# Kernel optimization log

Hardware: AMD Instinct MI355X
Metric: run time of the kernel (lower is better)

The kernel has to match this reference:

```python
import jax, jax.numpy as jnp
import numpy as np

D_MODEL = 1024
N_HEAD = 16
B, T = 1, 4096


def setup_inputs() -> dict:
    key = jax.random.key(0)
    ks = jax.random.split(key, 12)
    s = 1.0 / np.sqrt(D_MODEL)
    inp = {
        "q": jax.random.normal(ks[0], (B, T, D_MODEL), jnp.float32),
        "k": jax.random.normal(ks[1], (B, T, D_MODEL), jnp.float32),
        "v": jax.random.normal(ks[2], (B, T, D_MODEL), jnp.float32),
        # causal mask: True = keep, False = mask out (mask==0 path in torch)
        "mask": jnp.tril(jnp.ones((T, T), dtype=bool))[None, None],
        "w_q": jax.random.uniform(ks[3], (D_MODEL, D_MODEL), jnp.float32, -s, s),
        "b_q": jax.random.uniform(ks[4], (D_MODEL,), jnp.float32, -s, s),
        "w_k": jax.random.uniform(ks[5], (D_MODEL, D_MODEL), jnp.float32, -s, s),
        "b_k": jax.random.uniform(ks[6], (D_MODEL,), jnp.float32, -s, s),
        "w_v": jax.random.uniform(ks[7], (D_MODEL, D_MODEL), jnp.float32, -s, s),
        "b_v": jax.random.uniform(ks[8], (D_MODEL,), jnp.float32, -s, s),
        "w_o": jax.random.uniform(ks[9], (D_MODEL, D_MODEL), jnp.float32, -s, s),
        "b_o": jax.random.uniform(ks[10], (D_MODEL,), jnp.float32, -s, s),
    }
    return inp


def reference(q, k, v, mask, w_q, b_q, w_k, b_k, w_v, b_v, w_o, b_o):
    batch, time, d_model = q.shape
    n_d = d_model // N_HEAD
    # Linear projections (torch Linear: x @ W.T + b)
    qh = (q @ w_q.T + b_q).reshape(batch, time, N_HEAD, n_d).transpose(0, 2, 1, 3)
    kh = (k @ w_k.T + b_k).reshape(batch, -1, N_HEAD, n_d).transpose(0, 2, 1, 3)
    vh = (v @ w_v.T + b_v).reshape(batch, -1, N_HEAD, n_d).transpose(0, 2, 1, 3)
    # [B, H, Tq, Tk] score matrix (naive, materialized as in original)
    score = jnp.einsum("bhqd,bhkd->bhqk", qh, kh) / jnp.sqrt(jnp.float32(n_d))
    score = jnp.where(mask, score, jnp.float32(-10000.0))
    attn = jax.nn.softmax(score, axis=-1)
    out = jnp.einsum("bhqk,bhkd->bhqd", attn, vh)
    out = out.transpose(0, 2, 1, 3).reshape(batch, time, d_model)
    return out @ w_o.T + b_o
```

## Files before the change

### kernel.cpp

```cpp
#include <hip/hip_runtime.h>

typedef unsigned short u16;
typedef unsigned int u32;
typedef __bf16 b16x8 __attribute__((ext_vector_type(8)));
typedef float f32x4 __attribute__((ext_vector_type(4)));
typedef u32 u32x4 __attribute__((ext_vector_type(4)));

__device__ __forceinline__ u16 f2b(float f) {
    u32 u = __builtin_bit_cast(u32, f);
    u32 r = (u + 0x7fffu + ((u >> 16) & 1u)) >> 16;
    return (u16)r;
}
__device__ __forceinline__ float b2f(u16 h) {
    u32 u = ((u32)h) << 16;
    return __builtin_bit_cast(float, u);
}
__device__ __forceinline__ b16x8 frag(u32x4 x) { return __builtin_bit_cast(b16x8, x); }

__device__ __forceinline__ void gld16(const u16* g, u16* l) {
    __builtin_amdgcn_global_load_lds((const __attribute__((address_space(1))) u32*)g,
                                     (__attribute__((address_space(3))) u32*)l, 16, 0, 0);
}

#define SEQ 4096
#define DMODEL 1024
#define NHEAD 16
#define HDIM 64
#define QK_SCALE 0.18033688011112042f

__global__ void cvt3(const float* __restrict__ s0, const float* __restrict__ s1,
                     const float* __restrict__ s2, u16* __restrict__ d0,
                     u16* __restrict__ d1, u16* __restrict__ d2, int n4) {
    const int t = blockIdx.y;
    const float* s = (t == 0) ? s0 : (t == 1) ? s1 : s2;
    u16* d = (t == 0) ? d0 : (t == 1) ? d1 : d2;
    const int stride = gridDim.x * blockDim.x;
    for (int i = blockIdx.x * blockDim.x + threadIdx.x; i < n4; i += stride) {
        float4 f = ((const float4*)s)[i];
        ushort4 o;
        o.x = f2b(f.x); o.y = f2b(f.y); o.z = f2b(f.z); o.w = f2b(f.w);
        ((ushort4*)d)[i] = o;
    }
}

__global__ void cvt4(const float* __restrict__ s0, const float* __restrict__ s1,
                     const float* __restrict__ s2, const float* __restrict__ s3,
                     u16* __restrict__ d0, u16* __restrict__ d1,
                     u16* __restrict__ d2, u16* __restrict__ d3, int n4) {
    const int t = blockIdx.y;
    const float* s = (t == 0) ? s0 : (t == 1) ? s1 : (t == 2) ? s2 : s3;
    u16* d = (t == 0) ? d0 : (t == 1) ? d1 : (t == 2) ? d2 : d3;
    const int stride = gridDim.x * blockDim.x;
    for (int i = blockIdx.x * blockDim.x + threadIdx.x; i < n4; i += stride) {
        float4 f = ((const float4*)s)[i];
        ushort4 o;
        o.x = f2b(f.x); o.y = f2b(f.y); o.z = f2b(f.z); o.w = f2b(f.w);
        ((ushort4*)d)[i] = o;
    }
}

__global__ __launch_bounds__(256) void gemm_qkv(
    const u16* __restrict__ cq, const u16* __restrict__ ck, const u16* __restrict__ cv,
    const u16* __restrict__ cwq, const u16* __restrict__ cwk, const u16* __restrict__ cwv,
    const float* __restrict__ bq, const float* __restrict__ bk, const float* __restrict__ bv,
    u16* __restrict__ qh, u16* __restrict__ kh, u16* __restrict__ vt) {
    constexpr int K = 1024;
    __shared__ __attribute__((aligned(16))) u16 As[128 * 32];
    __shared__ __attribute__((aligned(16))) u16 Bs[128 * 32];

    const int z = blockIdx.z;
    const u16* A = (z == 0) ? cq : (z == 1) ? ck : cwv;
    const u16* Bt = (z == 0) ? cwq : (z == 1) ? cwk : cv;
    const float* bias = (z == 0) ? bq : (z == 1) ? bk : bv;

    int m0, n0;
    if (z < 2) {
        m0 = blockIdx.y * 128;
        n0 = blockIdx.x * 128;
    } else {
        const int id = blockIdx.y * 8 + blockIdx.x;
        m0 = (id >> 5) * 128;
        n0 = (id & 31) * 128;
    }

    const int tid = threadIdx.x;
    const int wave = tid >> 6, lane = tid & 63;
    const int quad = lane >> 4, l16 = lane & 15;
    const int wr = wave >> 1, wc = wave & 1;

    f32x4 acc[4][4] = {};

    const int srow = tid >> 2;
    const int scol = (tid & 3) * 8;
    const u16* Aptr = A + (size_t)(m0 + srow) * K + scol;
    const u16* Bptr = Bt + (size_t)(n0 + srow) * K + scol;
    u16* AsW0 = &As[wave * 512];
    u16* AsW1 = &As[2048 + wave * 512];
    u16* BsW0 = &Bs[wave * 512];
    u16* BsW1 = &Bs[2048 + wave * 512];

    for (int k0 = 0; k0 < K; k0 += 32) {
        __syncthreads();
        gld16(Aptr + k0, AsW0);
        gld16(Aptr + k0 + (size_t)64 * K, AsW1);
        gld16(Bptr + k0, BsW0);
        gld16(Bptr + k0 + (size_t)64 * K, BsW1);
        __syncthreads();

        b16x8 af[4], bf[4];
#pragma unroll
        for (int mt = 0; mt < 4; ++mt)
            af[mt] = frag(*(const u32x4*)&As[(wr * 64 + mt * 16 + l16) * 32 + quad * 8]);
#pragma unroll
        for (int nt = 0; nt < 4; ++nt)
            bf[nt] = frag(*(const u32x4*)&Bs[(wc * 64 + nt * 16 + l16) * 32 + quad * 8]);
#pragma unroll
        for (int mt = 0; mt < 4; ++mt)
#pragma unroll
            for (int nt = 0; nt < 4; ++nt)
                acc[mt][nt] = __builtin_amdgcn_mfma_f32_16x16x32_bf16(af[mt], bf[nt], acc[mt][nt], 0, 0, 0);
    }

    u16* C = (z == 0) ? qh : kh;
    const float sc = (z == 0) ? QK_SCALE : 1.0f;
#pragma unroll
    for (int nt = 0; nt < 4; ++nt) {
        const int col = n0 + wc * 64 + nt * 16 + l16;
        const float bcol = (z < 2) ? bias[col] : 0.f;
#pragma unroll
        for (int mt = 0; mt < 4; ++mt) {
            const int row0 = m0 + wr * 64 + mt * 16 + quad * 4;
#pragma unroll
            for (int r = 0; r < 4; ++r) {
                const int row = row0 + r;
                float v = acc[mt][nt][r];
                if (z == 2) {
                    v += bias[row];
                    vt[(size_t)row * SEQ + col] = f2b(v);
                } else {
                    v = (v + bcol) * sc;
                    C[((size_t)(col >> 6) * SEQ + row) * HDIM + (col & 63)] = f2b(v);
                }
            }
        }
    }
}

__global__ __launch_bounds__(256) void gemm_out(const u16* __restrict__ A,
                                                const u16* __restrict__ Bt,
                                                const float* __restrict__ bias,
                                                float* __restrict__ C) {
    constexpr int K = 1024, N = 1024;
    __shared__ __attribute__((aligned(16))) u16 As[128 * 32];
    __shared__ __attribute__((aligned(16))) u16 Bs[64 * 32];

    const int tid = threadIdx.x;
    const int wave = tid >> 6, lane = tid & 63;
    const int quad = lane >> 4, l16 = lane & 15;
    const int wr = wave >> 1, wc = wave & 1;
    const int m0 = blockIdx.y * 128, n0 = blockIdx.x * 64;

    f32x4 acc[4][2] = {};

    const int srow = tid >> 2;
    const int scol = (tid & 3) * 8;
    const u16* Aptr = A + (size_t)(m0 + srow) * K + scol;
    const u16* Bptr = Bt + (size_t)(n0 + wave * 16 + (lane >> 2)) * K + (lane & 3) * 8;
    u16* AsW0 = &As[wave * 512];
    u16* AsW1 = &As[2048 + wave * 512];
    u16* BsW = &Bs[wave * 512];

    for (int k0 = 0; k0 < K; k0 += 32) {
        __syncthreads();
        gld16(Aptr + k0, AsW0);
        gld16(Aptr + k0 + (size_t)64 * K, AsW1);
        gld16(Bptr + k0, BsW);
        __syncthreads();

        b16x8 af[4], bf[2];
#pragma unroll
        for (int mt = 0; mt < 4; ++mt)
            af[mt] = frag(*(const u32x4*)&As[(wr * 64 + mt * 16 + l16) * 32 + quad * 8]);
#pragma unroll
        for (int nt = 0; nt < 2; ++nt)
            bf[nt] = frag(*(const u32x4*)&Bs[(wc * 32 + nt * 16 + l16) * 32 + quad * 8]);
#pragma unroll
        for (int mt = 0; mt < 4; ++mt)
#pragma unroll
            for (int nt = 0; nt < 2; ++nt)
                acc[mt][nt] = __builtin_amdgcn_mfma_f32_16x16x32_bf16(af[mt], bf[nt], acc[mt][nt], 0, 0, 0);
    }

#pragma unroll
    for (int nt = 0; nt < 2; ++nt) {
        const int col = n0 + wc * 32 + nt * 16 + l16;
        const float bv = bias[col];
#pragma unroll
        for (int mt = 0; mt < 4; ++mt) {
            const int row0 = m0 + wr * 64 + mt * 16 + quad * 4;
#pragma unroll
            for (int r = 0; r < 4; ++r)
                C[(size_t)(row0 + r) * N + col] = acc[mt][nt][r] + bv;
        }
    }
}

__global__ __launch_bounds__(256) void flash_attn(const u16* __restrict__ Q,
                                                  const u16* __restrict__ K,
                                                  const u16* __restrict__ V,
                                                  u16* __restrict__ pO,
                                                  float* __restrict__ pL) {
    constexpr int LDK = 72;
    __shared__ __attribute__((aligned(16))) u16 Ks[64 * LDK];
    __shared__ __attribute__((aligned(16))) u16 Vs[64 * LDK];
    __shared__ __attribute__((aligned(16))) u16 Ps[128 * LDK];

    const int tid = threadIdx.x;
    const int wave = tid >> 6, lane = tid & 63;
    const int quad = lane >> 4, l16 = lane & 15;

    const int x = blockIdx.x, h = blockIdx.y;
    int qt, c, nc;
    if (x < 8)       { qt = x;                 c = 0;            nc = 1; }
    else if (x < 24) { qt = 8 + ((x - 8) >> 1);  c = (x - 8) & 1;  nc = 2; }
    else if (x < 48) { qt = 16 + (x - 24) / 3;   c = (x - 24) % 3; nc = 3; }
    else             { qt = 24 + ((x - 48) >> 2); c = (x - 48) & 3; nc = 4; }
    const int nkt = 2 * qt + 2;
    const int kt0 = (c * nkt) / nc, kt1 = ((c + 1) * nkt) / nc;
    const int q0 = qt * 128;
    const int slot = h * 80 + x;

    const u16* Qh = Q + (size_t)h * SEQ * HDIM;
    const u16* Kh = K + (size_t)h * SEQ * HDIM;
    const u16* Vh = V + (size_t)h * HDIM * SEQ;

    b16x8 qf[2][2];
#pragma unroll
    for (int mf = 0; mf < 2; ++mf) {
        const u16* qp = Qh + (size_t)(q0 + wave * 32 + mf * 16 + l16) * HDIM + quad * 8;
        qf[mf][0] = frag(*(const u32x4*)qp);
        qf[mf][1] = frag(*(const u32x4*)(qp + 32));
    }
    b16x8 onesf;
    {
        u32x4 o = {0x3F803F80u, 0x3F803F80u, 0x3F803F80u, 0x3F803F80u};
        onesf = frag(o);
    }

    f32x4 acc[2][4] = {};
    f32x4 accl[2] = {};

    const int r0 = tid >> 3;
    const int c0 = (tid & 7) * 8;

    for (int kt = kt0; kt < kt1; ++kt) {
        const int k0 = kt * 64;
        u32x4 ka = *(const u32x4*)(Kh + (size_t)(k0 + r0) * HDIM + c0);
        u32x4 kb = *(const u32x4*)(Kh + (size_t)(k0 + r0 + 32) * HDIM + c0);
        u32x4 va = *(const u32x4*)(Vh + (size_t)r0 * SEQ + k0 + c0);
        u32x4 vb = *(const u32x4*)(Vh + (size_t)(r0 + 32) * SEQ + k0 + c0);
        __syncthreads();
        *(u32x4*)&Ks[r0 * LDK + c0] = ka;
        *(u32x4*)&Ks[(r0 + 32) * LDK + c0] = kb;
        *(u32x4*)&Vs[r0 * LDK + c0] = va;
        *(u32x4*)&Vs[(r0 + 32) * LDK + c0] = vb;
        __syncthreads();

        f32x4 s[2][4];
#pragma unroll
        for (int nt = 0; nt < 4; ++nt) {
            b16x8 kf0 = frag(*(const u32x4*)&Ks[(nt * 16 + l16) * LDK + quad * 8]);
            b16x8 kf1 = frag(*(const u32x4*)&Ks[(nt * 16 + l16) * LDK + 32 + quad * 8]);
#pragma unroll
            for (int mf = 0; mf < 2; ++mf) {
                f32x4 z = {};
                z = __builtin_amdgcn_mfma_f32_16x16x32_bf16(qf[mf][0], kf0, z, 0, 0, 0);
                z = __builtin_amdgcn_mfma_f32_16x16x32_bf16(qf[mf][1], kf1, z, 0, 0, 0);
                s[mf][nt] = z;
            }
        }

        if (kt >= 2 * qt) {
#pragma unroll
            for (int nt = 0; nt < 4; ++nt) {
                const int j = k0 + nt * 16 + l16;
#pragma unroll
                for (int mf = 0; mf < 2; ++mf) {
                    const int ib = q0 + wave * 32 + mf * 16 + quad * 4;
#pragma unroll
                    for (int r = 0; r < 4; ++r)
                        if (j > ib + r) s[mf][nt][r] = -1e30f;
                }
            }
        }

#pragma unroll
        for (int mf = 0; mf < 2; ++mf)
#pragma unroll
            for (int nt = 0; nt < 4; ++nt)
#pragma unroll
                for (int r = 0; r < 4; ++r) {
                    const float p = __builtin_amdgcn_exp2f(s[mf][nt][r] - 16.0f);
                    Ps[(wave * 32 + mf * 16 + quad * 4 + r) * LDK + nt * 16 + l16] = f2b(p);
                }
        __syncthreads();

#pragma unroll
        for (int ks = 0; ks < 2; ++ks) {
            b16x8 a[2];
#pragma unroll
            for (int mf = 0; mf < 2; ++mf) {
                a[mf] = frag(*(const u32x4*)&Ps[(wave * 32 + mf * 16 + l16) * LDK + ks * 32 + quad * 8]);
                accl[mf] = __builtin_amdgcn_mfma_f32_16x16x32_bf16(a[mf], onesf, accl[mf], 0, 0, 0);
            }
#pragma unroll
            for (int dt = 0; dt < 4; ++dt) {
                b16x8 b = frag(*(const u32x4*)&Vs[(dt * 16 + l16) * LDK + ks * 32 + quad * 8]);
#pragma unroll
                for (int mf = 0; mf < 2; ++mf)
                    acc[mf][dt] = __builtin_amdgcn_mfma_f32_16x16x32_bf16(a[mf], b, acc[mf][dt], 0, 0, 0);
            }
        }
    }

    u16* po = pO + (size_t)slot * 8192;
#pragma unroll
    for (int mf = 0; mf < 2; ++mf) {
        const int row0 = wave * 32 + mf * 16 + quad * 4;
#pragma unroll
        for (int dt = 0; dt < 4; ++dt) {
            const int col = dt * 16 + l16;
            ushort4 o;
            o.x = f2b(acc[mf][dt][0]);
            o.y = f2b(acc[mf][dt][1]);
            o.z = f2b(acc[mf][dt][2]);
            o.w = f2b(acc[mf][dt][3]);
            *(ushort4*)&po[col * 128 + row0] = o;
        }
        if (l16 == 0) {
#pragma unroll
            for (int r = 0; r < 4; ++r)
                pL[(size_t)slot * 128 + row0 + r] = accl[mf][r];
        }
    }
}

__global__ __launch_bounds__(256) void combine(const u16* __restrict__ pO,
                                               const float* __restrict__ pL,
                                               u16* __restrict__ att) {
    const int qt = blockIdx.x, h = blockIdx.y;
    const int g = qt >> 3;
    const int nc = g + 1;
    const int slot0 = h * 80 + 4 * g * (g + 1) + (qt - (g << 3)) * nc;

    const int t = threadIdx.x;
    const int row = t >> 1;
    const int ch = (t & 1) * 32;

    float lsum = 0.f;
    for (int cc = 0; cc < nc; ++cc) lsum += pL[(size_t)(slot0 + cc) * 128 + row];
    const float inv = 1.0f / lsum;

    u16 out[32];
#pragma unroll 4
    for (int i = 0; i < 32; ++i) {
        const int col = ch + i;
        float o = 0.f;
        for (int cc = 0; cc < nc; ++cc)
            o += b2f(pO[(size_t)(slot0 + cc) * 8192 + col * 128 + row]);
        out[i] = f2b(o * inv);
    }
    u16* dst = att + (size_t)(qt * 128 + row) * DMODEL + h * HDIM + ch;
#pragma unroll
    for (int i = 0; i < 8; ++i) ((ushort4*)dst)[i] = *(ushort4*)&out[i * 4];
}

extern "C" void kernel_launch(void* const* d_in, const int* in_sizes, int n_in,
                              void* d_out, int out_size, void* d_ws, size_t ws_size,
                              hipStream_t stream) {
    const float* qkv[3] = {nullptr, nullptr, nullptr};
    const float* wts[4] = {nullptr, nullptr, nullptr, nullptr};
    const float* bss[4] = {nullptr, nullptr, nullptr, nullptr};
    int nqkv = 0, nw = 0, nb = 0;
    for (int i = 0; i < n_in; ++i) {
        const int sz = in_sizes[i];
        if (sz == SEQ * DMODEL) {
            if (nqkv < 3) qkv[nqkv++] = (const float*)d_in[i];
        } else if (sz == DMODEL * DMODEL) {
            if (nw < 4) wts[nw++] = (const float*)d_in[i];
        } else if (sz == DMODEL) {
            if (nb < 4) bss[nb++] = (const float*)d_in[i];
        }
    }

    u16* ws = (u16*)d_ws;
    const size_t ELEMS = (size_t)SEQ * DMODEL;
    const size_t WELEMS = (size_t)DMODEL * DMODEL;

    size_t off = 0;
    u16* cq = ws + off; off += ELEMS;
    u16* ck = ws + off; off += ELEMS;
    u16* cv = ws + off; off += ELEMS;
    u16* cwq = ws + off; off += WELEMS;
    u16* cwk = ws + off; off += WELEMS;
    u16* cwv = ws + off; off += WELEMS;
    u16* cwo = ws + off; off += WELEMS;
    u16* qh = ws + off; off += ELEMS;
    u16* kh = ws + off; off += ELEMS;
    u16* vt = ws + off; off += ELEMS;
    u16* att = ws + off; off += ELEMS;
    u16* pO = cq;
    float* pL = (float*)cwq;

    dim3 blk(256);
    cvt3<<<dim3(1024, 3), blk, 0, stream>>>(qkv[0], qkv[1], qkv[2], cq, ck, cv,
                                            (int)(ELEMS / 4));
    cvt4<<<dim3(256, 4), blk, 0, stream>>>(wts[0], wts[1], wts[2], wts[3],
                                           cwq, cwk, cwv, cwo, (int)(WELEMS / 4));

    gemm_qkv<<<dim3(8, 32, 3), blk, 0, stream>>>(cq, ck, cv, cwq, cwk, cwv,
                                                 bss[0], bss[1], bss[2], qh, kh, vt);
    flash_attn<<<dim3(80, NHEAD), blk, 0, stream>>>(qh, kh, vt, pO, pL);
    combine<<<dim3(SEQ / 128, NHEAD), blk, 0, stream>>>(pO, pL, att);
    gemm_out<<<dim3(16, 32), blk, 0, stream>>>(att, cwo, bss[3], (float*)d_out);
}
```

Measured before the change: 368.7 us.

## Double-buffer GEMM LDS tiles, prefetch K/V in attention, reorder attention blocks

The QKV and output GEMMs now use two LDS buffers, so the next 32-wide K slice loads into the second buffer while MFMAs run on the first. This halves the barrier pairs per K step at the cost of twice the shared memory. Flash attention loads the next K/V tile into registers while computing the current one, and drops the barrier after writing P, since each wave reads only its own P rows. Block indices are reversed so the longest causal query tiles are scheduled first, which should reduce tail imbalance.

```diff
diff --git a/kernel.cpp b/kernel.cpp
--- a/kernel.cpp
+++ b/kernel.cpp
@@ -59,14 +59,26 @@
     }
 }
 
+#define GEMM_PHASE(AS, BS)                                                                  \
+    {                                                                                       \
+        b16x8 af[4], bf[4];                                                                 \
+        _Pragma("unroll") for (int mt = 0; mt < 4; ++mt) af[mt] =                           \
+            frag(*(const u32x4*)&(AS)[(wr * 64 + mt * 16 + l16) * 32 + quad * 8]);          \
+        _Pragma("unroll") for (int nt = 0; nt < 4; ++nt) bf[nt] =                           \
+            frag(*(const u32x4*)&(BS)[(wc * 64 + nt * 16 + l16) * 32 + quad * 8]);          \
+        _Pragma("unroll") for (int mt = 0; mt < 4; ++mt)                                    \
+            _Pragma("unroll") for (int nt = 0; nt < 4; ++nt) acc[mt][nt] =                  \
+                __builtin_amdgcn_mfma_f32_16x16x32_bf16(af[mt], bf[nt], acc[mt][nt], 0, 0, 0); \
+    }
+
 __global__ __launch_bounds__(256) void gemm_qkv(
     const u16* __restrict__ cq, const u16* __restrict__ ck, const u16* __restrict__ cv,
     const u16* __restrict__ cwq, const u16* __restrict__ cwk, const u16* __restrict__ cwv,
     const float* __restrict__ bq, const float* __restrict__ bk, const float* __restrict__ bv,
     u16* __restrict__ qh, u16* __restrict__ kh, u16* __restrict__ vt) {
     constexpr int K = 1024;
-    __shared__ __attribute__((aligned(16))) u16 As[128 * 32];
-    __shared__ __attribute__((aligned(16))) u16 Bs[128 * 32];
+    __shared__ __attribute__((aligned(16))) u16 As[2][128 * 32];
+    __shared__ __attribute__((aligned(16))) u16 Bs[2][128 * 32];
 
     const int z = blockIdx.z;
     const u16* A = (z == 0) ? cq : (z == 1) ? ck : cwv;
@@ -94,31 +106,32 @@
     const int scol = (tid & 3) * 8;
     const u16* Aptr = A + (size_t)(m0 + srow) * K + scol;
     const u16* Bptr = Bt + (size_t)(n0 + srow) * K + scol;
-    u16* AsW0 = &As[wave * 512];
-    u16* AsW1 = &As[2048 + wave * 512];
-    u16* BsW0 = &Bs[wave * 512];
-    u16* BsW1 = &Bs[2048 + wave * 512];
-
-    for (int k0 = 0; k0 < K; k0 += 32) {
-        __syncthreads();
-        gld16(Aptr + k0, AsW0);
-        gld16(Aptr + k0 + (size_t)64 * K, AsW1);
-        gld16(Bptr + k0, BsW0);
-        gld16(Bptr + k0 + (size_t)64 * K, BsW1);
-        __syncthreads();
-
-        b16x8 af[4], bf[4];
-#pragma unroll
-        for (int mt = 0; mt < 4; ++mt)
-            af[mt] = frag(*(const u32x4*)&As[(wr * 64 + mt * 16 + l16) * 32 + quad * 8]);
-#pragma unroll
-        for (int nt = 0; nt < 4; ++nt)
-            bf[nt] = frag(*(const u32x4*)&Bs[(wc * 64 + nt * 16 + l16) * 32 + quad * 8]);
-#pragma unroll
-        for (int mt = 0; mt < 4; ++mt)
-#pragma unroll
-            for (int nt = 0; nt < 4; ++nt)
-                acc[mt][nt] = __builtin_amdgcn_mfma_f32_16x16x32_bf16(af[mt], bf[nt], acc[mt][nt], 0, 0, 0);
+    const int woff = wave * 512;
+
+    gld16(Aptr, &As[0][woff]);
+    gld16(Aptr + (size_t)64 * K, &As[0][2048 + woff]);
+    gld16(Bptr, &Bs[0][woff]);
+    gld16(Bptr + (size_t)64 * K, &Bs[0][2048 + woff]);
+
+    for (int k0 = 0; k0 < K; k0 += 64) {
+        __syncthreads();
+        {
+            const int kn = k0 + 32;
+            gld16(Aptr + kn, &As[1][woff]);
+            gld16(Aptr + kn + (size_t)64 * K, &As[1][2048 + woff]);
+            gld16(Bptr + kn, &Bs[1][woff]);
+            gld16(Bptr + kn + (size_t)64 * K, &Bs[1][2048 + woff]);
+        }
+        GEMM_PHASE(As[0], Bs[0]);
+        __syncthreads();
+        if (k0 + 64 < K) {
+            const int kn = k0 + 64;
+            gld16(Aptr + kn, &As[0][woff]);
+            gld16(Aptr + kn + (size_t)64 * K, &As[0][2048 + woff]);
+            gld16(Bptr + kn, &Bs[0][woff]);
+            gld16(Bptr + kn + (size_t)64 * K, &Bs[0][2048 + woff]);
+        }
+        GEMM_PHASE(As[1], Bs[1]);
     }
 
     u16* C = (z == 0) ? qh : kh;
@@ -151,8 +164,8 @@
                                                 const float* __restrict__ bias,
                                                 float* __restrict__ C) {
     constexpr int K = 1024, N = 1024;
-    __shared__ __attribute__((aligned(16))) u16 As[128 * 32];
-    __shared__ __attribute__((aligned(16))) u16 Bs[64 * 32];
+    __shared__ __attribute__((aligned(16))) u16 As[2][128 * 32];
+    __shared__ __attribute__((aligned(16))) u16 Bs[2][64 * 32];
 
     const int tid = threadIdx.x;
     const int wave = tid >> 6, lane = tid & 63;
@@ -166,29 +179,41 @@
     const int scol = (tid & 3) * 8;
     const u16* Aptr = A + (size_t)(m0 + srow) * K + scol;
     const u16* Bptr = Bt + (size_t)(n0 + wave * 16 + (lane >> 2)) * K + (lane & 3) * 8;
-    u16* AsW0 = &As[wave * 512];
-    u16* AsW1 = &As[2048 + wave * 512];
-    u16* BsW = &Bs[wave * 512];
-
-    for (int k0 = 0; k0 < K; k0 += 32) {
-        __syncthreads();
-        gld16(Aptr + k0, AsW0);
-        gld16(Aptr + k0 + (size_t)64 * K, AsW1);
-        gld16(Bptr + k0, BsW);
-        __syncthreads();
-
-        b16x8 af[4], bf[2];
-#pragma unroll
-        for (int mt = 0; mt < 4; ++mt)
-            af[mt] = frag(*(const u32x4*)&As[(wr * 64 + mt * 16 + l16) * 32 + quad * 8]);
-#pragma unroll
-        for (int nt = 0; nt < 2; ++nt)
-            bf[nt] = frag(*(const u32x4*)&Bs[(wc * 32 + nt * 16 + l16) * 32 + quad * 8]);
-#pragma unroll
-        for (int mt = 0; mt < 4; ++mt)
-#pragma unroll
-            for (int nt = 0; nt < 2; ++nt)
-                acc[mt][nt] = __builtin_amdgcn_mfma_f32_16x16x32_bf16(af[mt], bf[nt], acc[mt][nt], 0, 0, 0);
+    const int woff = wave * 512;
+
+    gld16(Aptr, &As[0][woff]);
+    gld16(Aptr + (size_t)64 * K, &As[0][2048 + woff]);
+    gld16(Bptr, &Bs[0][woff]);
+
+#define OUT_PHASE(AS, BS)                                                                   \
+    {                                                                                       \
+        b16x8 af[4], bf[2];                                                                 \
+        _Pragma("unroll") for (int mt = 0; mt < 4; ++mt) af[mt] =                           \
+            frag(*(const u32x4*)&(AS)[(wr * 64 + mt * 16 + l16) * 32 + quad * 8]);          \
+        _Pragma("unroll") for (int nt = 0; nt < 2; ++nt) bf[nt] =                           \
+            frag(*(const u32x4*)&(BS)[(wc * 32 + nt * 16 + l16) * 32 + quad * 8]);          \
+        _Pragma("unroll") for (int mt = 0; mt < 4; ++mt)                                    \
+            _Pragma("unroll") for (int nt = 0; nt < 2; ++nt) acc[mt][nt] =                  \
+                __builtin_amdgcn_mfma_f32_16x16x32_bf16(af[mt], bf[nt], acc[mt][nt], 0, 0, 0); \
+    }
+
+    for (int k0 = 0; k0 < K; k0 += 64) {
+        __syncthreads();
+        {
+            const int kn = k0 + 32;
+            gld16(Aptr + kn, &As[1][woff]);
+            gld16(Aptr + kn + (size_t)64 * K, &As[1][2048 + woff]);
+            gld16(Bptr + kn, &Bs[1][woff]);
+        }
+        OUT_PHASE(As[0], Bs[0]);
+        __syncthreads();
+        if (k0 + 64 < K) {
+            const int kn = k0 + 64;
+            gld16(Aptr + kn, &As[0][woff]);
+            gld16(Aptr + kn + (size_t)64 * K, &As[0][2048 + woff]);
+            gld16(Bptr + kn, &Bs[0][woff]);
+        }
+        OUT_PHASE(As[1], Bs[1]);
     }
 
 #pragma unroll
@@ -219,9 +244,9 @@
     const int wave = tid >> 6, lane = tid & 63;
     const int quad = lane >> 4, l16 = lane & 15;
 
-    const int x = blockIdx.x, h = blockIdx.y;
+    const int x = 79 - blockIdx.x, h = blockIdx.y;
     int qt, c, nc;
-    if (x < 8)       { qt = x;                 c = 0;            nc = 1; }
+    if (x < 8)       { qt = x;                   c = 0;            nc = 1; }
     else if (x < 24) { qt = 8 + ((x - 8) >> 1);  c = (x - 8) & 1;  nc = 2; }
     else if (x < 48) { qt = 16 + (x - 24) / 3;   c = (x - 24) % 3; nc = 3; }
     else             { qt = 24 + ((x - 48) >> 2); c = (x - 48) & 3; nc = 4; }
@@ -253,18 +278,30 @@
     const int r0 = tid >> 3;
     const int c0 = (tid & 7) * 8;
 
+    u32x4 ka, kb, va, vb;
+    {
+        const int k0 = kt0 * 64;
+        ka = *(const u32x4*)(Kh + (size_t)(k0 + r0) * HDIM + c0);
+        kb = *(const u32x4*)(Kh + (size_t)(k0 + r0 + 32) * HDIM + c0);
+        va = *(const u32x4*)(Vh + (size_t)r0 * SEQ + k0 + c0);
+        vb = *(const u32x4*)(Vh + (size_t)(r0 + 32) * SEQ + k0 + c0);
+    }
+
     for (int kt = kt0; kt < kt1; ++kt) {
         const int k0 = kt * 64;
-        u32x4 ka = *(const u32x4*)(Kh + (size_t)(k0 + r0) * HDIM + c0);
-        u32x4 kb = *(const u32x4*)(Kh + (size_t)(k0 + r0 + 32) * HDIM + c0);
-        u32x4 va = *(const u32x4*)(Vh + (size_t)r0 * SEQ + k0 + c0);
-        u32x4 vb = *(const u32x4*)(Vh + (size_t)(r0 + 32) * SEQ + k0 + c0);
         __syncthreads();
         *(u32x4*)&Ks[r0 * LDK + c0] = ka;
         *(u32x4*)&Ks[(r0 + 32) * LDK + c0] = kb;
         *(u32x4*)&Vs[r0 * LDK + c0] = va;
         *(u32x4*)&Vs[(r0 + 32) * LDK + c0] = vb;
         __syncthreads();
+        if (kt + 1 < kt1) {
+            const int kn = (kt + 1) * 64;
+            ka = *(const u32x4*)(Kh + (size_t)(kn + r0) * HDIM + c0);
+            kb = *(const u32x4*)(Kh + (size_t)(kn + r0 + 32) * HDIM + c0);
+            va = *(const u32x4*)(Vh + (size_t)r0 * SEQ + kn + c0);
+            vb = *(const u32x4*)(Vh + (size_t)(r0 + 32) * SEQ + kn + c0);
+        }
 
         f32x4 s[2][4];
 #pragma unroll
@@ -303,7 +340,6 @@
                     const float p = __builtin_amdgcn_exp2f(s[mf][nt][r] - 16.0f);
                     Ps[(wave * 32 + mf * 16 + quad * 4 + r) * LDK + nt * 16 + l16] = f2b(p);
                 }
-        __syncthreads();
 
 #pragma unroll
         for (int ks = 0; ks < 2; ++ks) {
```

Measured after the change: 383.0 us. 1.04x slower.

## Rebalance attention key splits, reverse block order, and vectorize P stores

Applied to the files above, without the earlier changes.

Replaces the fixed 80-slot split with 102 slots per head, where the number of key chunks per query tile grows every six tiles. Blocks are launched heaviest-first to improve load balance across CUs. The QK MFMA operands are swapped so each lane holds four consecutive keys of one query row. This lets P be written to LDS as ushort4 vectors, and the barrier before the PV step is dropped because each wave reads only the rows it wrote. The combine indexing and the pL workspace location are updated to fit the larger partial-output buffer.

```diff
diff --git a/kernel.cpp b/kernel.cpp
--- a/kernel.cpp
+++ b/kernel.cpp
@@ -27,6 +27,7 @@
 #define NHEAD 16
 #define HDIM 64
 #define QK_SCALE 0.18033688011112042f
+#define SLOTS_PER_HEAD 102
 
 __global__ void cvt3(const float* __restrict__ s0, const float* __restrict__ s1,
                      const float* __restrict__ s2, u16* __restrict__ d0,
@@ -219,16 +220,19 @@
     const int wave = tid >> 6, lane = tid & 63;
     const int quad = lane >> 4, l16 = lane & 15;
 
-    const int x = blockIdx.x, h = blockIdx.y;
-    int qt, c, nc;
-    if (x < 8)       { qt = x;                 c = 0;            nc = 1; }
-    else if (x < 24) { qt = 8 + ((x - 8) >> 1);  c = (x - 8) & 1;  nc = 2; }
-    else if (x < 48) { qt = 16 + (x - 24) / 3;   c = (x - 24) % 3; nc = 3; }
-    else             { qt = 24 + ((x - 48) >> 2); c = (x - 48) & 3; nc = 4; }
+    const int xx = (SLOTS_PER_HEAD - 1) - blockIdx.x;
+    const int h = blockIdx.y;
+    int qt = 0, base = 0, nc = 1;
+    for (; qt < 32; ++qt) {
+        nc = (qt + 6) / 6;
+        if (xx < base + nc) break;
+        base += nc;
+    }
+    const int c = xx - base;
     const int nkt = 2 * qt + 2;
     const int kt0 = (c * nkt) / nc, kt1 = ((c + 1) * nkt) / nc;
     const int q0 = qt * 128;
-    const int slot = h * 80 + x;
+    const int slot = h * SLOTS_PER_HEAD + xx;
 
     const u16* Qh = Q + (size_t)h * SEQ * HDIM;
     const u16* Kh = K + (size_t)h * SEQ * HDIM;
@@ -266,7 +270,7 @@
         *(u32x4*)&Vs[(r0 + 32) * LDK + c0] = vb;
         __syncthreads();
 
-        f32x4 s[2][4];
+        f32x4 st[2][4];
 #pragma unroll
         for (int nt = 0; nt < 4; ++nt) {
             b16x8 kf0 = frag(*(const u32x4*)&Ks[(nt * 16 + l16) * LDK + quad * 8]);
@@ -274,22 +278,22 @@
 #pragma unroll
             for (int mf = 0; mf < 2; ++mf) {
                 f32x4 z = {};
-                z = __builtin_amdgcn_mfma_f32_16x16x32_bf16(qf[mf][0], kf0, z, 0, 0, 0);
-                z = __builtin_amdgcn_mfma_f32_16x16x32_bf16(qf[mf][1], kf1, z, 0, 0, 0);
-                s[mf][nt] = z;
+                z = __builtin_amdgcn_mfma_f32_16x16x32_bf16(kf0, qf[mf][0], z, 0, 0, 0);
+                z = __builtin_amdgcn_mfma_f32_16x16x32_bf16(kf1, qf[mf][1], z, 0, 0, 0);
+                st[mf][nt] = z;
             }
         }
 
         if (kt >= 2 * qt) {
 #pragma unroll
             for (int nt = 0; nt < 4; ++nt) {
-                const int j = k0 + nt * 16 + l16;
+                const int keyb = k0 + nt * 16 + quad * 4;
 #pragma unroll
                 for (int mf = 0; mf < 2; ++mf) {
-                    const int ib = q0 + wave * 32 + mf * 16 + quad * 4;
+                    const int qrow = q0 + wave * 32 + mf * 16 + l16;
 #pragma unroll
                     for (int r = 0; r < 4; ++r)
-                        if (j > ib + r) s[mf][nt][r] = -1e30f;
+                        if (keyb + r > qrow) st[mf][nt][r] = -1e30f;
                 }
             }
         }
@@ -297,13 +301,14 @@
 #pragma unroll
         for (int mf = 0; mf < 2; ++mf)
 #pragma unroll
-            for (int nt = 0; nt < 4; ++nt)
-#pragma unroll
-                for (int r = 0; r < 4; ++r) {
-                    const float p = __builtin_amdgcn_exp2f(s[mf][nt][r] - 16.0f);
-                    Ps[(wave * 32 + mf * 16 + quad * 4 + r) * LDK + nt * 16 + l16] = f2b(p);
-                }
-        __syncthreads();
+            for (int nt = 0; nt < 4; ++nt) {
+                ushort4 o;
+                o.x = f2b(__builtin_amdgcn_exp2f(st[mf][nt][0] - 16.0f));
+                o.y = f2b(__builtin_amdgcn_exp2f(st[mf][nt][1] - 16.0f));
+                o.z = f2b(__builtin_amdgcn_exp2f(st[mf][nt][2] - 16.0f));
+                o.w = f2b(__builtin_amdgcn_exp2f(st[mf][nt][3] - 16.0f));
+                *(ushort4*)&Ps[(wave * 32 + mf * 16 + l16) * LDK + nt * 16 + quad * 4] = o;
+            }
 
 #pragma unroll
         for (int ks = 0; ks < 2; ++ks) {
@@ -349,9 +354,9 @@
                                                const float* __restrict__ pL,
                                                u16* __restrict__ att) {
     const int qt = blockIdx.x, h = blockIdx.y;
-    const int g = qt >> 3;
-    const int nc = g + 1;
-    const int slot0 = h * 80 + 4 * g * (g + 1) + (qt - (g << 3)) * nc;
+    const int g = qt / 6;
+    const int nc = (qt + 6) / 6;
+    const int slot0 = h * SLOTS_PER_HEAD + qt + 3 * g * (g - 1) + (qt - 6 * g) * g;
 
     const int t = threadIdx.x;
     const int row = t >> 1;
@@ -410,7 +415,7 @@
     u16* vt = ws + off; off += ELEMS;
     u16* att = ws + off; off += ELEMS;
     u16* pO = cq;
-    float* pL = (float*)cwq;
+    float* pL = (float*)cwk;
 
     dim3 blk(256);
     cvt3<<<dim3(1024, 3), blk, 0, stream>>>(qkv[0], qkv[1], qkv[2], cq, ck, cv,
@@ -420,7 +425,7 @@
 
     gemm_qkv<<<dim3(8, 32, 3), blk, 0, stream>>>(cq, ck, cv, cwq, cwk, cwv,
                                                  bss[0], bss[1], bss[2], qh, kh, vt);
-    flash_attn<<<dim3(80, NHEAD), blk, 0, stream>>>(qh, kh, vt, pO, pL);
+    flash_attn<<<dim3(SLOTS_PER_HEAD, NHEAD), blk, 0, stream>>>(qh, kh, vt, pO, pL);
     combine<<<dim3(SEQ / 128, NHEAD), blk, 0, stream>>>(pO, pL, att);
     gemm_out<<<dim3(16, 32), blk, 0, stream>>>(att, cwo, bss[3], (float*)d_out);
 }
```

New measurement: 373.9 us. No clear change (+1.4%).
